# Performance work log

Hardware: AMD Instinct MI355X
Metric: run time of the kernel (lower is better)

The kernel has to match this reference:

```python
import jax, jax.numpy as jnp
import numpy as np

B, H, W, C = 2, 48, 48, 768
HEADS, HD = 12, 64
MLP = 3072
BOT = 384


def ln(x, w, b, eps=1e-5):
    mu = x.mean(-1, keepdims=True)
    var = ((x - mu) ** 2).mean(-1, keepdims=True)
    return (x - mu) * jax.lax.rsqrt(var + eps) * w + b


def ln_chan(x, w, b, eps=1e-6):
    # detectron2-style LayerNorm over channel dim for NCHW tensors
    mu = x.mean(1, keepdims=True)
    var = ((x - mu) ** 2).mean(1, keepdims=True)
    return (x - mu) * jax.lax.rsqrt(var + eps) * w[None, :, None, None] + b[None, :, None, None]


def conv(x, w, pad):
    return jax.lax.conv_general_dilated(x, w, (1, 1), [(pad, pad), (pad, pad)],
                                        dimension_numbers=('NCHW', 'OIHW', 'NCHW'))


def setup_inputs() -> dict:
    key = jax.random.key(0)
    ks = jax.random.split(key, 32)
    r = lambda i, shape, s=0.02: (jax.random.normal(ks[i], shape) * s).astype(jnp.float32)
    return {
        'x': jax.random.normal(ks[0], (B, H, W, C), dtype=jnp.float32),
        'norm1_w': jnp.ones((C,), jnp.float32), 'norm1_b': jnp.zeros((C,), jnp.float32),
        'qkv_w': r(1, (C, 3 * C)), 'qkv_b': r(2, (3 * C,)),
        'proj_w': r(3, (C, C)), 'proj_b': r(4, (C,)),
        'rel_pos_h': r(5, (2 * H - 1, HD)), 'rel_pos_w': r(6, (2 * W - 1, HD)),
        'norm2_w': jnp.ones((C,), jnp.float32), 'norm2_b': jnp.zeros((C,), jnp.float32),
        'fc1_w': r(7, (C, MLP)), 'fc1_b': r(8, (MLP,)),
        'fc2_w': r(9, (MLP, C)), 'fc2_b': r(10, (C,)),
        'conv1_w': r(11, (BOT, C, 1, 1)), 'rln1_w': jnp.ones((BOT,), jnp.float32), 'rln1_b': jnp.zeros((BOT,), jnp.float32),
        'conv2_w': r(12, (BOT, BOT, 3, 3)), 'rln2_w': jnp.ones((BOT,), jnp.float32), 'rln2_b': jnp.zeros((BOT,), jnp.float32),
        'conv3_w': r(13, (C, BOT, 1, 1)), 'rln3_w': r(14, (C,)), 'rln3_b': r(15, (C,)),
    }


def reference(x, norm1_w, norm1_b, qkv_w, qkv_b, proj_w, proj_b, rel_pos_h, rel_pos_w,
              norm2_w, norm2_b, fc1_w, fc1_b, fc2_w, fc2_b,
              conv1_w, rln1_w, rln1_b, conv2_w, rln2_w, rln2_b, conv3_w, rln3_w, rln3_b):
    b, h, w, c = x.shape
    hd = c // HEADS
    n = h * w
    scale = hd ** -0.5

    shortcut = x
    xn = ln(x, norm1_w, norm1_b)
    # qkv projection: (B,N,3,heads,hd) -> (3, B*heads, N, hd)
    qkv = (xn.reshape(b, n, c) @ qkv_w + qkv_b).reshape(b, n, 3, HEADS, hd)
    qkv = qkv.transpose(2, 0, 3, 1, 4).reshape(3, b * HEADS, n, hd)
    q, k, v = qkv[0], qkv[1], qkv[2]

    attn = jnp.einsum('bnd,bmd->bnm', q * scale, k)  # (B*heads, N, N)

    # decomposed relative position bias
    idx_h = jnp.arange(h)[:, None] - jnp.arange(h)[None, :] + (h - 1)
    idx_w = jnp.arange(w)[:, None] - jnp.arange(w)[None, :] + (w - 1)
    Rh = rel_pos_h[idx_h]  # (H, H, hd)
    Rw = rel_pos_w[idx_w]  # (W, W, hd)
    rq = q.reshape(b * HEADS, h, w, hd)
    rel_h = jnp.einsum('bhwc,hkc->bhwk', rq, Rh)
    rel_w = jnp.einsum('bhwc,wkc->bhwk', rq, Rw)
    attn = attn.reshape(b * HEADS, h, w, h, w) + rel_h[:, :, :, :, None] + rel_w[:, :, :, None, :]
    attn = jax.nn.softmax(attn.reshape(b * HEADS, n, n), axis=-1)

    out = (attn @ v).reshape(b, HEADS, h, w, hd).transpose(0, 2, 3, 1, 4).reshape(b, h, w, c)
    x = shortcut + (out @ proj_w + proj_b)

    # MLP
    xn = ln(x, norm2_w, norm2_b)
    hdn = jax.nn.gelu(xn @ fc1_w + fc1_b, approximate=False)
    x = x + (hdn @ fc2_w + fc2_b)

    # residual bottleneck block (NCHW)
    y = x.transpose(0, 3, 1, 2)
    o = jax.nn.gelu(ln_chan(conv(y, conv1_w, 0), rln1_w, rln1_b), approximate=False)
    o = jax.nn.gelu(ln_chan(conv(o, conv2_w, 1), rln2_w, rln2_b), approximate=False)
    o = ln_chan(conv(o, conv3_w, 0), rln3_w, rln3_b)
    y = y + o
    return y.transpose(0, 2, 3, 1)
```

## Files before the change

kernel.cpp:

```cpp
#include <hip/hip_runtime.h>

typedef unsigned short ushort_t;
typedef __attribute__((ext_vector_type(8))) short bf16x8;
typedef __attribute__((ext_vector_type(4))) float f32x4;

#define DEV static __device__ __forceinline__

DEV ushort_t f2bf(float f){
  union { float f; unsigned u; } v; v.f = f;
  unsigned r = v.u + 0x7FFFu + ((v.u >> 16) & 1u);
  return (ushort_t)(r >> 16);
}
DEV float bf2f(ushort_t h){
  union { unsigned u; float f; } v; v.u = ((unsigned)h) << 16;
  return v.f;
}
DEV float gelu_f(float x){ return 0.5f * x * (1.f + erff(x * 0.70710678118654752f)); }

#define MFMA16(a,b,c) __builtin_amdgcn_mfma_f32_16x16x32_bf16((a),(b),(c),0,0,0)

DEV void gld16(const ushort_t* g, ushort_t* l){
  __builtin_amdgcn_global_load_lds(
      (const __attribute__((address_space(1))) unsigned int*)g,
      (__attribute__((address_space(3))) unsigned int*)l, 16, 0, 0);
}


__global__ __launch_bounds__(256) void transpose_all_kernel(
    const float* __restrict__ s0, const float* __restrict__ s1,
    const float* __restrict__ s2, const float* __restrict__ s3,
    ushort_t* __restrict__ d0, ushort_t* __restrict__ d1,
    ushort_t* __restrict__ d2, ushort_t* __restrict__ d3){
  __shared__ float tile[32][33];
  int b = blockIdx.x;
  const float* src; ushort_t* dst; int K, N, bx, by;
  if(b < 1728){ src=s0; dst=d0; K=768;  N=2304; bx=b%24;          by=b/24; }
  else if(b < 2304){ int c=b-1728; src=s1; dst=d1; K=768;  N=768;  bx=c%24; by=c/24; }
  else if(b < 4608){ int c=b-2304; src=s2; dst=d2; K=768;  N=3072; bx=c%24; by=c/24; }
  else             { int c=b-4608; src=s3; dst=d3; K=3072; N=768;  bx=c%96; by=c/96; }
  int k0 = bx*32, n0 = by*32;
  int tx = threadIdx.x & 31, ty = threadIdx.x >> 5;
  #pragma unroll
  for(int i = ty; i < 32; i += 8) tile[i][tx] = src[(long)(k0+i)*N + n0 + tx];
  __syncthreads();
  #pragma unroll
  for(int i = ty; i < 32; i += 8) dst[(long)(n0+i)*K + k0 + tx] = f2bf(tile[tx][i]);
}

__global__ void cast_all_kernel(
    const float* __restrict__ c1w, const float* __restrict__ c2w,
    const float* __restrict__ c3w, const float* __restrict__ rph,
    const float* __restrict__ rpw,
    ushort_t* __restrict__ wc1, ushort_t* __restrict__ wc2,
    ushort_t* __restrict__ wc3, ushort_t* __restrict__ tabh,
    ushort_t* __restrict__ tabw){
  int i = blockIdx.x*256 + threadIdx.x;
  if(i < 294912){ wc1[i] = f2bf(c1w[i]); }
  else if(i < 1622016){
    int j = i - 294912;
    int co = j / 3456, r = j - co*3456;
    int dy = r / 1152; int r2 = r - dy*1152;
    int dx = r2 / 384; int ci = r2 - dx*384;
    wc2[j] = f2bf(c2w[((co*384 + ci)*3 + dy)*3 + dx]);
  }
  else if(i < 1916928){ int j = i - 1622016; wc3[j] = f2bf(c3w[j]); }
  else if(i < 1923008){ int j = i - 1916928; tabh[j] = f2bf(rph[j]); }
  else if(i < 1929088){ int j = i - 1923008; tabw[j] = f2bf(rpw[j]); }
}

__global__ __launch_bounds__(256) void vt_kernel(
    const ushort_t* __restrict__ v, ushort_t* __restrict__ vt){
  __shared__ __align__(16) ushort_t t[64][72];
  int bh = blockIdx.y, nt = blockIdx.x;
  int tid = threadIdx.x;
  #pragma unroll
  for(int p=0;p<2;p++){
    int item = tid + p*256;
    int tok = item >> 3, ch = item & 7;
    bf16x8 vv = *(const bf16x8*)(v + ((long)(bh*2304 + nt*64 + tok))*64 + ch*8);
    #pragma unroll
    for(int j=0;j<8;j++) t[ch*8+j][tok] = (ushort_t)vv[j];
  }
  __syncthreads();
  #pragma unroll
  for(int p=0;p<2;p++){
    int item = tid + p*256;
    int d = item >> 3, c2 = item & 7;
    bf16x8 rd = *(const bf16x8*)&t[d][c2*8];
    *(bf16x8*)(vt + ((long)(bh*64 + d))*2304 + nt*64 + c2*8) = rd;
  }
}

template<int D, bool GELU, bool RES, bool PADOUT>
__global__ __launch_bounds__(256) void ln_kernel(
    const float* __restrict__ in, const float* __restrict__ w, const float* __restrict__ bv,
    const float* __restrict__ res, float eps,
    ushort_t* __restrict__ outb, float* __restrict__ outf){
  constexpr int PER = D/64;
  int lane = threadIdx.x & 63, wid = threadIdx.x >> 6;
  long row = (long)blockIdx.x*4 + wid;
  const float* ip = in + row*D;
  float x[PER]; float s = 0.f;
  #pragma unroll
  for(int i=0;i<PER;i++){ x[i] = ip[i*64 + lane]; s += x[i]; }
  #pragma unroll
  for(int o=32;o>=1;o>>=1) s += __shfl_xor(s, o);
  float mu = s * (1.f/D);
  float vs = 0.f;
  #pragma unroll
  for(int i=0;i<PER;i++){ float d = x[i]-mu; vs += d*d; }
  #pragma unroll
  for(int o=32;o>=1;o>>=1) vs += __shfl_xor(vs, o);
  float rstd = rsqrtf(vs*(1.f/D) + eps);
  long obase;
  if constexpr(PADOUT){
    int bb = (int)(row / 2304); int rm = (int)(row - (long)bb*2304);
    int y = rm / 48, xx = rm - y*48;
    obase = ((long)((bb*50 + y+1)*50) + (xx+1))*384;
  } else obase = row*D;
  #pragma unroll
  for(int i=0;i<PER;i++){
    int c = i*64 + lane;
    float y = (x[i]-mu)*rstd*w[c] + bv[c];
    if constexpr(GELU) y = gelu_f(y);
    if constexpr(RES)  y += res[row*D + c];
    if(outb) outb[obase + c] = f2bf(y);
    if(outf) outf[row*D + c] = y;
  }
}

__global__ __launch_bounds__(256) void relpos_mfma_kernel(
    const ushort_t* __restrict__ q, const ushort_t* __restrict__ tabh,
    const ushort_t* __restrict__ tabw,
    float* __restrict__ relh, float* __restrict__ relw){
  const int bh = blockIdx.y;
  const bool isH = (blockIdx.z == 0);
  const int w = threadIdx.x >> 6, lane = threadIdx.x & 63;
  const int la = lane & 15, grp = lane >> 4;
  const int pos0 = blockIdx.x*4 + w;
  const ushort_t* tab = isH ? tabh : tabw;
  float* outp = isH ? relh : relw;
  const ushort_t* qbase = q + (long)bh*2304*64;

  bf16x8 bf0[3], bf1[3];
  #pragma unroll
  for(int ni=0;ni<3;ni++){
    int dpos = pos0 - (ni*16+la) + 47;
    const ushort_t* tp = tab + dpos*64 + grp*8;
    bf0[ni] = *(const bf16x8*)tp;
    bf1[ni] = *(const bf16x8*)(tp+32);
  }
  #pragma unroll
  for(int mi=0;mi<3;mi++){
    int arow = mi*16 + la;
    long na = isH ? ((long)pos0*48 + arow) : ((long)arow*48 + pos0);
    const ushort_t* qp = qbase + na*64 + grp*8;
    bf16x8 a0 = *(const bf16x8*)qp;
    bf16x8 a1 = *(const bf16x8*)(qp+32);
    f32x4 c[3];
    #pragma unroll
    for(int ni=0;ni<3;ni++){
      f32x4 z; z[0]=0.f; z[1]=0.f; z[2]=0.f; z[3]=0.f;
      z = MFMA16(a0, bf0[ni], z);
      z = MFMA16(a1, bf1[ni], z);
      c[ni] = z;
    }
    #pragma unroll
    for(int ni=0;ni<3;ni++)
      #pragma unroll
      for(int r=0;r<4;r++){
        int orow = mi*16 + grp*4 + r;
        long no = isH ? ((long)pos0*48 + orow) : ((long)orow*48 + pos0);
        outp[((long)bh*2304 + no)*48 + ni*16 + la] = c[ni][r] * 8.0f;
      }
  }
}

template<int BM, int EPI, bool IM2COL>
__global__ __launch_bounds__(256) void gemm_kernel(
    const ushort_t* __restrict__ A, const ushort_t* __restrict__ Wt,
    const float* __restrict__ bias, const float* __restrict__ res,
    float* __restrict__ outf, ushort_t* __restrict__ ob0,
    ushort_t* __restrict__ ob1, ushort_t* __restrict__ ob2,
    int N, int Kdim){
  constexpr int FR = BM/32;
  __shared__ __align__(16) ushort_t Asm[BM*64];
  __shared__ __align__(16) ushort_t Bsm[BM*64];
  const int tid = threadIdx.x, lane = tid & 63, w = tid >> 6;
  const int wm = w >> 1, wn = w & 1;
  const int la = lane & 15, grp = lane >> 4;
  const int m0 = blockIdx.y * BM, n0 = blockIdx.x * BM;
  f32x4 acc[FR][FR];
  #pragma unroll
  for(int i=0;i<FR;i++)
    #pragma unroll
    for(int j=0;j<FR;j++)
      #pragma unroll
      for(int r=0;r<4;r++) acc[i][j][r] = 0.f;

  const int srw = lane >> 3;
  const int scs = ((lane&7) ^ srw) * 8;
  for(int k0 = 0; k0 < Kdim; k0 += 64){
    if(k0) __syncthreads();
    #pragma unroll
    for(int t=0;t<FR;t++){
      int r = w*(BM/4) + t*8 + srw;
      const ushort_t* ga;
      if constexpr(IM2COL){
        int m = m0 + r;
        int bb = m / 2304; int rm = m - bb*2304;
        int y = rm / 48, x = rm - y*48;
        int dy = k0 / 1152; int r2 = k0 - dy*1152;
        int dx = r2 / 384;  int cb = r2 - dx*384;
        ga = A + (((long)((bb*50 + y+dy)*50) + (x+dx))*384 + cb + scs);
      } else {
        ga = A + (long)(m0+r)*Kdim + k0 + scs;
      }
      gld16(ga, &Asm[(w*(BM/4)+t*8)*64]);
      gld16(Wt + (long)(n0+r)*Kdim + k0 + scs, &Bsm[(w*(BM/4)+t*8)*64]);
    }
    __syncthreads();
    #pragma unroll
    for(int ks=0; ks<2; ks++){
      bf16x8 af[FR], bfm[FR];
      #pragma unroll
      for(int mi=0;mi<FR;mi++){
        int row = wm*(BM/2) + mi*16 + la;
        af[mi] = *(const bf16x8*)&Asm[row*64 + ((((ks<<2)+grp) ^ (row&7))*8)];
      }
      #pragma unroll
      for(int ni=0;ni<FR;ni++){
        int row = wn*(BM/2) + ni*16 + la;
        bfm[ni] = *(const bf16x8*)&Bsm[row*64 + ((((ks<<2)+grp) ^ (row&7))*8)];
      }
      #pragma unroll
      for(int mi=0;mi<FR;mi++)
        #pragma unroll
        for(int ni=0;ni<FR;ni++)
          acc[mi][ni] = MFMA16(af[mi], bfm[ni], acc[mi][ni]);
    }
  }
  #pragma unroll
  for(int mi=0;mi<FR;mi++)
  #pragma unroll
  for(int ni=0;ni<FR;ni++)
  #pragma unroll
  for(int r=0;r<4;r++){
    int mm = m0 + wm*(BM/2) + mi*16 + grp*4 + r;
    int nn = n0 + wn*(BM/2) + ni*16 + la;
    float v = acc[mi][ni][r];
    if constexpr(EPI == 0){
      outf[(long)mm*N + nn] = v;
    } else if constexpr(EPI == 1){
      v += bias[nn];
      int s = nn / 768; int rem = nn - s*768;
      int head = rem >> 6, d = rem & 63;
      if(s == 0) v *= 0.125f;
      int bb = mm / 2304; int nloc = mm - bb*2304;
      long idx = ((long)((bb*12+head)*2304 + nloc))*64 + d;
      ushort_t hv = f2bf(v);
      if(s == 0) ob0[idx] = hv; else if(s == 1) ob1[idx] = hv; else ob2[idx] = hv;
    } else if constexpr(EPI == 2){
      v += bias[nn] + res[(long)mm*N + nn];
      outf[(long)mm*N + nn] = v;
    } else if constexpr(EPI == 3){
      v = gelu_f(v + bias[nn]);
      ob0[(long)mm*N + nn] = f2bf(v);
    } else if constexpr(EPI == 4){
      v += bias[nn] + res[(long)mm*N + nn];
      outf[(long)mm*N + nn] = v;
      ob0[(long)mm*N + nn] = f2bf(v);
    }
  }
}

#define NSPLIT 2
#define NTS 18
__global__ __launch_bounds__(512) void attn_kernel(
    const ushort_t* __restrict__ Q, const ushort_t* __restrict__ Kb,
    const ushort_t* __restrict__ VT, const float* __restrict__ relh,
    const float* __restrict__ relw, float* __restrict__ Opart,
    float* __restrict__ mpart, float* __restrict__ lpart){
  __shared__ __align__(16) ushort_t Kl[2][64*64];
  __shared__ __align__(16) ushort_t Vl[2][64*64];
  const int bh = blockIdx.y, qt = blockIdx.x, sp = blockIdx.z;
  const int tid = threadIdx.x, lane = tid & 63, w = tid >> 6;
  const int la = lane & 15, grp = lane >> 4;
  const int qg = qt*128 + w*16 + la;
  const long row = (long)bh*2304 + qg;
  const int key0 = sp*NTS*64;

  const ushort_t* qp = Q + row*64 + grp*8;
  const bf16x8 qa0 = *(const bf16x8*)qp;
  const bf16x8 qa1 = *(const bf16x8*)(qp + 32);

  const ushort_t* kg = Kb + ((long)bh*2304 + key0)*64;
  const ushort_t* vg = VT + (long)bh*64*2304 + key0;
  const float* rhq = relh + row*48;

  f32x4 rw4[3];
  {
    const float* rwq = relw + row*48 + grp*4;
    #pragma unroll
    for(int c=0;c<3;c++) rw4[c] = *(const f32x4*)(rwq + 16*c);
  }

  const int srw = lane >> 3;
  const int scs = ((lane&7) ^ srw) * 8;
  const int strow = w*8 + srw;

  f32x4 acc[4];
  #pragma unroll
  for(int nf=0;nf<4;nf++){ acc[nf][0]=0.f; acc[nf][1]=0.f; acc[nf][2]=0.f; acc[nf][3]=0.f; }
  float m_run = -3e38f, l_run = 0.f;

  gld16(kg + (long)strow*64 + scs, &Kl[0][(w*8)*64]);
  gld16(vg + (long)strow*2304 + scs, &Vl[0][(w*8)*64]);

  for(int t=0; t<6; t++){
    #define ATTN_ITER(u)                                                         \
    {                                                                            \
      const int j = 3*t + (u);                                                   \
      const int cur = (t + (u)) & 1;                                             \
      asm volatile("s_waitcnt vmcnt(0)" ::: "memory");                           \
      __builtin_amdgcn_sched_barrier(0);                                         \
      __builtin_amdgcn_s_barrier();                                              \
      __builtin_amdgcn_sched_barrier(0);                                         \
      const int h0 = sp*24 + 4*t + (u);                                          \
      const float rha = rhq[h0];                                                 \
      const float rhb = rhq[h0+1];                                               \
      if(j+1 < NTS){                                                             \
        gld16(kg + ((long)((j+1)*64 + strow))*64 + scs, &Kl[cur^1][(w*8)*64]);   \
        gld16(vg + (long)strow*2304 + (j+1)*64 + scs, &Vl[cur^1][(w*8)*64]);     \
      }                                                                          \
      f32x4 s[4];                                                                \
      __builtin_amdgcn_s_setprio(1);                                             \
      _Pragma("unroll")                                                          \
      for(int nf=0;nf<4;nf++){                                                   \
        const ushort_t* kl = &Kl[cur][(nf*16+la)*64];                            \
        bf16x8 k0 = *(const bf16x8*)(kl + ((grp ^ (la&7))*8));                   \
        bf16x8 k1 = *(const bf16x8*)(kl + (((4+grp) ^ (la&7))*8));               \
        f32x4 z; z[0]=0.f; z[1]=0.f; z[2]=0.f; z[3]=0.f;                         \
        z = MFMA16(k0, qa0, z);                                                  \
        z = MFMA16(k1, qa1, z);                                                  \
        s[nf] = z;                                                               \
      }                                                                          \
      __builtin_amdgcn_s_setprio(0);                                             \
      float lmax = -3e38f;                                                       \
      _Pragma("unroll")                                                          \
      for(int nf=0;nf<4;nf++){                                                   \
        const int cp = (u) + nf;                                                 \
        const float rh = (cp >= 3) ? rhb : rha;                                  \
        const int c = (cp >= 3) ? cp-3 : cp;                                     \
        _Pragma("unroll")                                                        \
        for(int r=0;r<4;r++){                                                    \
          s[nf][r] += rh + rw4[c][r];                                            \
          lmax = fmaxf(lmax, s[nf][r]);                                          \
        }                                                                        \
      }                                                                          \
      lmax = fmaxf(lmax, __shfl_xor(lmax,16));                                   \
      lmax = fmaxf(lmax, __shfl_xor(lmax,32));                                   \
      const float mnew = fmaxf(m_run, lmax);                                     \
      const float alpha = __expf(m_run - mnew);                                  \
      m_run = mnew;                                                              \
      float psum = 0.f;                                                          \
      _Pragma("unroll")                                                          \
      for(int nf=0;nf<4;nf++)                                                    \
        _Pragma("unroll")                                                        \
        for(int r=0;r<4;r++){                                                    \
          s[nf][r] = __expf(s[nf][r] - mnew);                                    \
          psum += s[nf][r];                                                      \
        }                                                                        \
      psum += __shfl_xor(psum,16);                                               \
      psum += __shfl_xor(psum,32);                                               \
      l_run = l_run*alpha + psum;                                                \
      unsigned pk[4][2];                                                         \
      _Pragma("unroll")                                                          \
      for(int nf=0;nf<4;nf++)                                                    \
        _Pragma("unroll")                                                        \
        for(int h=0;h<2;h++)                                                     \
          asm("v_cvt_pk_bf16_f32 %0, %1, %2"                                     \
              : "=v"(pk[nf][h]) : "v"(s[nf][2*h]), "v"(s[nf][2*h+1]));           \
      _Pragma("unroll")                                                          \
      for(int nf=0;nf<4;nf++)                                                    \
        _Pragma("unroll")                                                        \
        for(int r=0;r<4;r++) acc[nf][r] *= alpha;                                \
      _Pragma("unroll")                                                          \
      for(int ks=0; ks<2; ks++){                                                 \
        unsigned wd[4];                                                          \
        _Pragma("unroll")                                                        \
        for(int j2=0;j2<4;j2++){                                                 \
          int src = la + 16*(((grp&1)<<1) + (j2>>1));                            \
          unsigned wA = __shfl(pk[2*ks  ][j2&1], src);                           \
          unsigned wB = __shfl(pk[2*ks+1][j2&1], src);                           \
          wd[j2] = (grp >= 2) ? wB : wA;                                         \
        }                                                                        \
        union { unsigned uu[4]; bf16x8 v; } pa;                                  \
        pa.uu[0]=wd[0]; pa.uu[1]=wd[1]; pa.uu[2]=wd[2]; pa.uu[3]=wd[3];          \
        __builtin_amdgcn_s_setprio(1);                                           \
        _Pragma("unroll")                                                        \
        for(int nf=0;nf<4;nf++){                                                 \
          const ushort_t* vl = &Vl[cur][(nf*16+la)*64];                          \
          bf16x8 vb = *(const bf16x8*)(vl + ((((ks<<2)+grp) ^ (la&7))*8));       \
          acc[nf] = MFMA16(vb, pa.v, acc[nf]);                                   \
        }                                                                        \
        __builtin_amdgcn_s_setprio(0);                                           \
      }                                                                          \
    }
    ATTN_ITER(0)
    ATTN_ITER(1)
    ATTN_ITER(2)
    #undef ATTN_ITER
  }

  float* op = Opart + ((long)sp*55296 + row)*64;
  #pragma unroll
  for(int nf=0;nf<4;nf++)
    *(f32x4*)(op + nf*16 + grp*4) = acc[nf];
  if(grp == 0){
    mpart[(long)sp*55296 + row] = m_run;
    lpart[(long)sp*55296 + row] = l_run;
  }
}

__global__ __launch_bounds__(256) void attn_merge_kernel(
    const float* __restrict__ Opart, const float* __restrict__ mpart,
    const float* __restrict__ lpart, ushort_t* __restrict__ outp){
  int wid = threadIdx.x >> 6, lane = threadIdx.x & 63;
  long row = (long)blockIdx.x*4 + wid;
  int bh = (int)(row / 2304); int n = (int)(row - (long)bh*2304);
  int b = bh / 12, head = bh - b*12;
  float m0 = mpart[row], m1 = mpart[55296+row];
  float ms = fmaxf(m0, m1);
  float w0 = __expf(m0-ms), w1 = __expf(m1-ms);
  float l = w0*lpart[row] + w1*lpart[55296+row];
  float o = w0*Opart[row*64+lane] + w1*Opart[(55296+row)*64+lane];
  outp[((long)b*2304+n)*768 + head*64 + lane] = f2bf(o / l);
}

extern "C" void kernel_launch(void* const* d_in, const int* in_sizes, int n_in,
                              void* d_out, int out_size, void* d_ws, size_t ws_size,
                              hipStream_t stream){
  const float* x     = (const float*)d_in[0];
  const float* n1w   = (const float*)d_in[1];
  const float* n1b   = (const float*)d_in[2];
  const float* qkvw  = (const float*)d_in[3];
  const float* qkvb  = (const float*)d_in[4];
  const float* projw = (const float*)d_in[5];
  const float* projb = (const float*)d_in[6];
  const float* rph   = (const float*)d_in[7];
  const float* rpw   = (const float*)d_in[8];
  const float* n2w   = (const float*)d_in[9];
  const float* n2b   = (const float*)d_in[10];
  const float* fc1w  = (const float*)d_in[11];
  const float* fc1b  = (const float*)d_in[12];
  const float* fc2w  = (const float*)d_in[13];
  const float* fc2b  = (const float*)d_in[14];
  const float* c1w   = (const float*)d_in[15];
  const float* r1w   = (const float*)d_in[16];
  const float* r1b   = (const float*)d_in[17];
  const float* c2w   = (const float*)d_in[18];
  const float* r2w   = (const float*)d_in[19];
  const float* r2b   = (const float*)d_in[20];
  const float* c3w   = (const float*)d_in[21];
  const float* r3w   = (const float*)d_in[22];
  const float* r3b   = (const float*)d_in[23];
  float* out = (float*)d_out;

  char* base = (char*)d_ws;
  size_t off = 0;
  auto carve = [&](size_t bytes)->char*{
    char* p = base + off;
    off += (bytes + 255) & ~(size_t)255;
    return p;
  };
  const long T = 4608;

  ushort_t* wqkvT = (ushort_t*)carve((size_t)2304*768*2);
  ushort_t* wprojT= (ushort_t*)carve((size_t)768*768*2);
  ushort_t* wfc1T = (ushort_t*)carve((size_t)3072*768*2);
  ushort_t* wfc2T = (ushort_t*)carve((size_t)768*3072*2);
  ushort_t* wc1   = (ushort_t*)carve((size_t)384*768*2);
  ushort_t* wc2   = (ushort_t*)carve((size_t)384*3456*2);
  ushort_t* wc3   = (ushort_t*)carve((size_t)768*384*2);
  ushort_t* tabhb = (ushort_t*)carve((size_t)95*64*2);
  ushort_t* tabwb = (ushort_t*)carve((size_t)95*64*2);
  ushort_t* xn1   = (ushort_t*)carve((size_t)T*768*2);
  ushort_t* qb    = (ushort_t*)carve((size_t)24*2304*64*2);
  ushort_t* kbuf  = (ushort_t*)carve((size_t)24*2304*64*2);
  ushort_t* vbuf  = (ushort_t*)carve((size_t)24*2304*64*2);
  ushort_t* vbufT = (ushort_t*)carve((size_t)24*2304*64*2);
  float*    relh  = (float*)carve((size_t)24*2304*48*4);
  float*    relw  = (float*)carve((size_t)24*2304*48*4);
  float*    Opart = (float*)carve((size_t)2*55296*64*4);
  float*    mpart = (float*)carve((size_t)2*55296*4);
  float*    lpart = (float*)carve((size_t)2*55296*4);
  ushort_t* attno = (ushort_t*)carve((size_t)T*768*2);
  float*    x1    = (float*)carve((size_t)T*768*4);
  ushort_t* xn2   = (ushort_t*)carve((size_t)T*768*2);
  ushort_t* hmlp  = (ushort_t*)carve((size_t)T*3072*2);
  float*    x2    = (float*)carve((size_t)T*768*4);
  ushort_t* x2b   = (ushort_t*)carve((size_t)T*768*2);
  float*    c1    = (float*)carve((size_t)T*384*4);
  ushort_t* o1pad = (ushort_t*)carve((size_t)2*50*50*384*2);
  float*    c2    = (float*)carve((size_t)T*384*4);
  ushort_t* o2    = (ushort_t*)carve((size_t)T*384*2);
  float*    c3    = (float*)carve((size_t)T*768*4);
  (void)ws_size; (void)in_sizes; (void)n_in; (void)out_size;

  transpose_all_kernel<<<dim3(6912),256,0,stream>>>(qkvw, projw, fc1w, fc2w,
                                                    wqkvT, wprojT, wfc1T, wfc2T);
  cast_all_kernel<<<dim3(7536),256,0,stream>>>(c1w, c2w, c3w, rph, rpw,
                                               wc1, wc2, wc3, tabhb, tabwb);
  hipMemsetAsync(o1pad, 0, (size_t)2*50*50*384*2, stream);

  ln_kernel<768,false,false,false><<<dim3(1152),256,0,stream>>>(x, n1w, n1b, nullptr, 1e-5f, xn1, nullptr);
  gemm_kernel<128,1,false><<<dim3(18,36),256,0,stream>>>(xn1, wqkvT, qkvb, nullptr, nullptr, qb, kbuf, vbuf, 2304, 768);
  vt_kernel<<<dim3(36,24),256,0,stream>>>(vbuf, vbufT);
  relpos_mfma_kernel<<<dim3(12,24,2),256,0,stream>>>(qb, tabhb, tabwb, relh, relw);
  attn_kernel<<<dim3(18,24,2),512,0,stream>>>(qb, kbuf, vbufT, relh, relw, Opart, mpart, lpart);
  attn_merge_kernel<<<dim3(13824),256,0,stream>>>(Opart, mpart, lpart, attno);
  gemm_kernel<64,2,false><<<dim3(12,72),256,0,stream>>>(attno, wprojT, projb, x, x1, nullptr, nullptr, nullptr, 768, 768);
  ln_kernel<768,false,false,false><<<dim3(1152),256,0,stream>>>(x1, n2w, n2b, nullptr, 1e-5f, xn2, nullptr);
  gemm_kernel<128,3,false><<<dim3(24,36),256,0,stream>>>(xn2, wfc1T, fc1b, nullptr, nullptr, hmlp, nullptr, nullptr, 3072, 768);
  gemm_kernel<64,4,false><<<dim3(12,72),256,0,stream>>>(hmlp, wfc2T, fc2b, x1, x2, x2b, nullptr, nullptr, 768, 3072);
  gemm_kernel<64,0,false><<<dim3(6,72),256,0,stream>>>(x2b, wc1, nullptr, nullptr, c1, nullptr, nullptr, nullptr, 384, 768);
  ln_kernel<384,true,false,true><<<dim3(1152),256,0,stream>>>(c1, r1w, r1b, nullptr, 1e-6f, o1pad, nullptr);
  gemm_kernel<64,0,true><<<dim3(6,72),256,0,stream>>>(o1pad, wc2, nullptr, nullptr, c2, nullptr, nullptr, nullptr, 384, 3456);
  ln_kernel<384,true,false,false><<<dim3(1152),256,0,stream>>>(c2, r2w, r2b, nullptr, 1e-6f, o2, nullptr);
  gemm_kernel<64,0,false><<<dim3(12,72),256,0,stream>>>(o2, wc3, nullptr, nullptr, c3, nullptr, nullptr, nullptr, 768, 384);
  ln_kernel<768,false,true,false><<<dim3(1152),256,0,stream>>>(c3, r3w, r3b, x2, 1e-6f, nullptr, out);
}
```

Before: 436.8 us.

## Use rectangular 64x128 GEMM tiles, lazy softmax rescale, drop setprio in attention

The GEMM kernel gets separate M and N tile sizes, and the smaller GEMMs now use 64x128 tiles, halving the grid along N. This is meant to raise B-operand reuse per block, at the cost of fewer blocks on a 256-CU device. The attention kernel now skips the online-softmax rescale of the accumulator unless the new row max exceeds the running max by more than 8, which saves exps and multiplies. It also removes the s_setprio hints around its MFMA sections.

```diff
diff --git a/kernel.cpp b/kernel.cpp
--- a/kernel.cpp
+++ b/kernel.cpp
@@ -176,25 +176,25 @@
   }
 }
 
-template<int BM, int EPI, bool IM2COL>
+template<int BM, int BN, int EPI, bool IM2COL>
 __global__ __launch_bounds__(256) void gemm_kernel(
     const ushort_t* __restrict__ A, const ushort_t* __restrict__ Wt,
     const float* __restrict__ bias, const float* __restrict__ res,
     float* __restrict__ outf, ushort_t* __restrict__ ob0,
     ushort_t* __restrict__ ob1, ushort_t* __restrict__ ob2,
     int N, int Kdim){
-  constexpr int FR = BM/32;
+  constexpr int FRm = BM/32, FRn = BN/32;
   __shared__ __align__(16) ushort_t Asm[BM*64];
-  __shared__ __align__(16) ushort_t Bsm[BM*64];
+  __shared__ __align__(16) ushort_t Bsm[BN*64];
   const int tid = threadIdx.x, lane = tid & 63, w = tid >> 6;
   const int wm = w >> 1, wn = w & 1;
   const int la = lane & 15, grp = lane >> 4;
-  const int m0 = blockIdx.y * BM, n0 = blockIdx.x * BM;
-  f32x4 acc[FR][FR];
-  #pragma unroll
-  for(int i=0;i<FR;i++)
-    #pragma unroll
-    for(int j=0;j<FR;j++)
+  const int m0 = blockIdx.y * BM, n0 = blockIdx.x * BN;
+  f32x4 acc[FRm][FRn];
+  #pragma unroll
+  for(int i=0;i<FRm;i++)
+    #pragma unroll
+    for(int j=0;j<FRn;j++)
       #pragma unroll
       for(int r=0;r<4;r++) acc[i][j][r] = 0.f;
 
@@ -203,7 +203,7 @@
   for(int k0 = 0; k0 < Kdim; k0 += 64){
     if(k0) __syncthreads();
     #pragma unroll
-    for(int t=0;t<FR;t++){
+    for(int t=0;t<FRm;t++){
       int r = w*(BM/4) + t*8 + srw;
       const ushort_t* ga;
       if constexpr(IM2COL){
@@ -217,37 +217,41 @@
         ga = A + (long)(m0+r)*Kdim + k0 + scs;
       }
       gld16(ga, &Asm[(w*(BM/4)+t*8)*64]);
-      gld16(Wt + (long)(n0+r)*Kdim + k0 + scs, &Bsm[(w*(BM/4)+t*8)*64]);
+    }
+    #pragma unroll
+    for(int t=0;t<FRn;t++){
+      int r = w*(BN/4) + t*8 + srw;
+      gld16(Wt + (long)(n0+r)*Kdim + k0 + scs, &Bsm[(w*(BN/4)+t*8)*64]);
     }
     __syncthreads();
     #pragma unroll
     for(int ks=0; ks<2; ks++){
-      bf16x8 af[FR], bfm[FR];
+      bf16x8 af[FRm], bfm[FRn];
       #pragma unroll
-      for(int mi=0;mi<FR;mi++){
+      for(int mi=0;mi<FRm;mi++){
         int row = wm*(BM/2) + mi*16 + la;
         af[mi] = *(const bf16x8*)&Asm[row*64 + ((((ks<<2)+grp) ^ (row&7))*8)];
       }
       #pragma unroll
-      for(int ni=0;ni<FR;ni++){
-        int row = wn*(BM/2) + ni*16 + la;
+      for(int ni=0;ni<FRn;ni++){
+        int row = wn*(BN/2) + ni*16 + la;
         bfm[ni] = *(const bf16x8*)&Bsm[row*64 + ((((ks<<2)+grp) ^ (row&7))*8)];
       }
       #pragma unroll
-      for(int mi=0;mi<FR;mi++)
+      for(int mi=0;mi<FRm;mi++)
         #pragma unroll
-        for(int ni=0;ni<FR;ni++)
+        for(int ni=0;ni<FRn;ni++)
           acc[mi][ni] = MFMA16(af[mi], bfm[ni], acc[mi][ni]);
     }
   }
   #pragma unroll
-  for(int mi=0;mi<FR;mi++)
-  #pragma unroll
-  for(int ni=0;ni<FR;ni++)
+  for(int mi=0;mi<FRm;mi++)
+  #pragma unroll
+  for(int ni=0;ni<FRn;ni++)
   #pragma unroll
   for(int r=0;r<4;r++){
     int mm = m0 + wm*(BM/2) + mi*16 + grp*4 + r;
-    int nn = n0 + wn*(BM/2) + ni*16 + la;
+    int nn = n0 + wn*(BN/2) + ni*16 + la;
     float v = acc[mi][ni][r];
     if constexpr(EPI == 0){
       outf[(long)mm*N + nn] = v;
@@ -334,7 +338,6 @@
         gld16(vg + (long)strow*2304 + (j+1)*64 + scs, &Vl[cur^1][(w*8)*64]);     \
       }                                                                          \
       f32x4 s[4];                                                                \
-      __builtin_amdgcn_s_setprio(1);                                             \
       _Pragma("unroll")                                                          \
       for(int nf=0;nf<4;nf++){                                                   \
         const ushort_t* kl = &Kl[cur][(nf*16+la)*64];                            \
@@ -345,7 +348,6 @@
         z = MFMA16(k1, qa1, z);                                                  \
         s[nf] = z;                                                               \
       }                                                                          \
-      __builtin_amdgcn_s_setprio(0);                                             \
       float lmax = -3e38f;                                                       \
       _Pragma("unroll")                                                          \
       for(int nf=0;nf<4;nf++){                                                   \
@@ -360,20 +362,27 @@
       }                                                                          \
       lmax = fmaxf(lmax, __shfl_xor(lmax,16));                                   \
       lmax = fmaxf(lmax, __shfl_xor(lmax,32));                                   \
-      const float mnew = fmaxf(m_run, lmax);                                     \
-      const float alpha = __expf(m_run - mnew);                                  \
-      m_run = mnew;                                                              \
+      if(!__all(lmax <= m_run + 8.f)){                                           \
+        const float mnew = fmaxf(m_run, lmax);                                   \
+        const float alpha = __expf(m_run - mnew);                                \
+        m_run = mnew;                                                            \
+        l_run *= alpha;                                                          \
+        _Pragma("unroll")                                                        \
+        for(int nf=0;nf<4;nf++)                                                  \
+          _Pragma("unroll")                                                      \
+          for(int r=0;r<4;r++) acc[nf][r] *= alpha;                              \
+      }                                                                          \
       float psum = 0.f;                                                          \
       _Pragma("unroll")                                                          \
       for(int nf=0;nf<4;nf++)                                                    \
         _Pragma("unroll")                                                        \
         for(int r=0;r<4;r++){                                                    \
-          s[nf][r] = __expf(s[nf][r] - mnew);                                    \
+          s[nf][r] = __expf(s[nf][r] - m_run);                                   \
           psum += s[nf][r];                                                      \
         }                                                                        \
       psum += __shfl_xor(psum,16);                                               \
       psum += __shfl_xor(psum,32);                                               \
-      l_run = l_run*alpha + psum;                                                \
+      l_run += psum;                                                             \
       unsigned pk[4][2];                                                         \
       _Pragma("unroll")                                                          \
       for(int nf=0;nf<4;nf++)                                                    \
@@ -381,10 +390,6 @@
         for(int h=0;h<2;h++)                                                     \
           asm("v_cvt_pk_bf16_f32 %0, %1, %2"                                     \
               : "=v"(pk[nf][h]) : "v"(s[nf][2*h]), "v"(s[nf][2*h+1]));           \
-      _Pragma("unroll")                                                          \
-      for(int nf=0;nf<4;nf++)                                                    \
-        _Pragma("unroll")                                                        \
-        for(int r=0;r<4;r++) acc[nf][r] *= alpha;                                \
       _Pragma("unroll")                                                          \
       for(int ks=0; ks<2; ks++){                                                 \
         unsigned wd[4];                                                          \
@@ -397,14 +402,12 @@
         }                                                                        \
         union { unsigned uu[4]; bf16x8 v; } pa;                                  \
         pa.uu[0]=wd[0]; pa.uu[1]=wd[1]; pa.uu[2]=wd[2]; pa.uu[3]=wd[3];          \
-        __builtin_amdgcn_s_setprio(1);                                           \
         _Pragma("unroll")                                                        \
         for(int nf=0;nf<4;nf++){                                                 \
           const ushort_t* vl = &Vl[cur][(nf*16+la)*64];                          \
           bf16x8 vb = *(const bf16x8*)(vl + ((((ks<<2)+grp) ^ (la&7))*8));       \
           acc[nf] = MFMA16(vb, pa.v, acc[nf]);                                   \
         }                                                                        \
-        __builtin_amdgcn_s_setprio(0);                                           \
       }                                                                          \
     }
     ATTN_ITER(0)
@@ -515,19 +518,19 @@
   hipMemsetAsync(o1pad, 0, (size_t)2*50*50*384*2, stream);
 
   ln_kernel<768,false,false,false><<<dim3(1152),256,0,stream>>>(x, n1w, n1b, nullptr, 1e-5f, xn1, nullptr);
-  gemm_kernel<128,1,false><<<dim3(18,36),256,0,stream>>>(xn1, wqkvT, qkvb, nullptr, nullptr, qb, kbuf, vbuf, 2304, 768);
+  gemm_kernel<128,128,1,false><<<dim3(18,36),256,0,stream>>>(xn1, wqkvT, qkvb, nullptr, nullptr, qb, kbuf, vbuf, 2304, 768);
   vt_kernel<<<dim3(36,24),256,0,stream>>>(vbuf, vbufT);
   relpos_mfma_kernel<<<dim3(12,24,2),256,0,stream>>>(qb, tabhb, tabwb, relh, relw);
   attn_kernel<<<dim3(18,24,2),512,0,stream>>>(qb, kbuf, vbufT, relh, relw, Opart, mpart, lpart);
   attn_merge_kernel<<<dim3(13824),256,0,stream>>>(Opart, mpart, lpart, attno);
-  gemm_kernel<64,2,false><<<dim3(12,72),256,0,stream>>>(attno, wprojT, projb, x, x1, nullptr, nullptr, nullptr, 768, 768);
+  gemm_kernel<64,128,2,false><<<dim3(6,72),256,0,stream>>>(attno, wprojT, projb, x, x1, nullptr, nullptr, nullptr, 768, 768);
   ln_kernel<768,false,false,false><<<dim3(1152),256,0,stream>>>(x1, n2w, n2b, nullptr, 1e-5f, xn2, nullptr);
-  gemm_kernel<128,3,false><<<dim3(24,36),256,0,stream>>>(xn2, wfc1T, fc1b, nullptr, nullptr, hmlp, nullptr, nullptr, 3072, 768);
-  gemm_kernel<64,4,false><<<dim3(12,72),256,0,stream>>>(hmlp, wfc2T, fc2b, x1, x2, x2b, nullptr, nullptr, 768, 3072);
-  gemm_kernel<64,0,false><<<dim3(6,72),256,0,stream>>>(x2b, wc1, nullptr, nullptr, c1, nullptr, nullptr, nullptr, 384, 768);
+  gemm_kernel<128,128,3,false><<<dim3(24,36),256,0,stream>>>(xn2, wfc1T, fc1b, nullptr, nullptr, hmlp, nullptr, nullptr, 3072, 768);
+  gemm_kernel<64,128,4,false><<<dim3(6,72),256,0,stream>>>(hmlp, wfc2T, fc2b, x1, x2, x2b, nullptr, nullptr, 768, 3072);
+  gemm_kernel<64,128,0,false><<<dim3(3,72),256,0,stream>>>(x2b, wc1, nullptr, nullptr, c1, nullptr, nullptr, nullptr, 384, 768);
   ln_kernel<384,true,false,true><<<dim3(1152),256,0,stream>>>(c1, r1w, r1b, nullptr, 1e-6f, o1pad, nullptr);
-  gemm_kernel<64,0,true><<<dim3(6,72),256,0,stream>>>(o1pad, wc2, nullptr, nullptr, c2, nullptr, nullptr, nullptr, 384, 3456);
+  gemm_kernel<64,128,0,true><<<dim3(3,72),256,0,stream>>>(o1pad, wc2, nullptr, nullptr, c2, nullptr, nullptr, nullptr, 384, 3456);
   ln_kernel<384,true,false,false><<<dim3(1152),256,0,stream>>>(c2, r2w, r2b, nullptr, 1e-6f, o2, nullptr);
-  gemm_kernel<64,0,false><<<dim3(12,72),256,0,stream>>>(o2, wc3, nullptr, nullptr, c3, nullptr, nullptr, nullptr, 768, 384);
+  gemm_kernel<64,128,0,false><<<dim3(6,72),256,0,stream>>>(o2, wc3, nullptr, nullptr, c3, nullptr, nullptr, nullptr, 768, 384);
   ln_kernel<768,false,true,false><<<dim3(1152),256,0,stream>>>(c3, r3w, r3b, x2, 1e-6f, nullptr, out);
 }
```

Measured after the change: 444.4 us. Within noise of the previous version (+1.8%).
